# Kernel tuning notes

Measured on AMD Instinct MI355X. Metric: run time of the kernel, lower is better.

The kernel has to match this reference:

```python
import jax, jax.numpy as jnp
import numpy as np

BATCH, T, MAXLEN, DMODEL = 8, 32, 8, 256
UNITS = MAXLEN * DMODEL  # 2048, GRU units == input_dim


def setup_inputs() -> dict:
    key = jax.random.key(0)
    k1, k2, k3, k4, k5 = jax.random.split(key, 5)
    scale = 1.0 / np.sqrt(UNITS)
    x = jax.random.normal(k1, (BATCH, T, MAXLEN, DMODEL), jnp.float32)
    h0 = jax.random.normal(k2, (BATCH, UNITS), jnp.float32) * 0.1
    W = jax.random.normal(k3, (UNITS, 3 * UNITS), jnp.float32) * scale  # input kernel
    U = jax.random.normal(k4, (UNITS, 3 * UNITS), jnp.float32) * scale  # recurrent kernel
    b = jax.random.normal(k5, (2, 3 * UNITS), jnp.float32) * 0.01  # [input_bias, recurrent_bias] (reset_after)
    return {"x": x, "h0": h0, "W": W, "U": U, "b": b}


def _gru_seq(xp, h0, U, b_rec):
    """Run GRU (Keras v2, reset_after=True) over precomputed input projections.
    xp: (B, T, 3U) = x @ W + b_in ; h0: (B, U). Returns ((B,T,U) states, (B,U) last)."""
    def step(h, xp_t):
        rec = h @ U + b_rec  # (B, 3U)
        xz, xr, xh = jnp.split(xp_t, 3, axis=-1)
        rz, rr, rh = jnp.split(rec, 3, axis=-1)
        z = jax.nn.sigmoid(xz + rz)
        r = jax.nn.sigmoid(xr + rr)
        hh = jnp.tanh(xh + r * rh)
        h_new = z * h + (1.0 - z) * hh
        return h_new, h_new
    h_last, hs = jax.lax.scan(step, h0, jnp.swapaxes(xp, 0, 1))
    return jnp.swapaxes(hs, 0, 1), h_last


def reference(x, h0, W, U, b):
    # x: (B, T, M, d). Causal branch: for each mask row i, zero out positions > i
    # along the maxLen axis, run the full-sequence GRU, keep slice i of output.
    B, T, M, d = x.shape
    units = M * d
    b_in, b_rec = b[0], b[1]
    masks = jnp.tril(jnp.ones((M, M), x.dtype))  # (M, M) lower triangular
    # Fold the M mask variants into the batch dim -> one fused scan.
    xm = (x[None] * masks[:, None, None, :, None]).reshape(M * B, T, units)
    xp = jnp.einsum('bti,iu->btu', xm, W) + b_in  # precompute input projection
    h0r = jnp.broadcast_to(h0[None], (M, B, units)).reshape(M * B, units)
    hs, h_last = _gru_seq(xp, h0r, U, b_rec)
    out = hs.reshape(M, B, T, M, d)
    idx = jnp.arange(M)
    ret = out[idx, :, :, idx, :]            # (M, B, T, d): slice i of variant i
    ret = jnp.transpose(ret, (1, 2, 0, 3))  # (B, T, M, d)
    state = h_last.reshape(M, B, units)[M - 1]  # state from last (full-mask) run
    return ret, state
```

## Files before the change

### kernel.cpp

```cpp
#include <hip/hip_runtime.h>
#include <hip/hip_bf16.h>

typedef _Float16 f16x8 __attribute__((ext_vector_type(8)));
typedef float f32x4 __attribute__((ext_vector_type(4)));
typedef unsigned long long ull;

#define UNITS   2048
#define NC      6144
#define TSTEPS  32
#define HSTRIDE 131072

__device__ __forceinline__ float sigmoid_f(float v){ return 1.0f/(1.0f+__expf(-v)); }
__device__ __forceinline__ float tanh_f(float v){ return 2.0f/(1.0f+__expf(-2.0f*v)) - 1.0f; }

__global__ __launch_bounds__(256) void prep_misc(
    const float* __restrict__ x, const float* __restrict__ h0,
    _Float16* __restrict__ xh, _Float16* __restrict__ hRing,
    unsigned* __restrict__ bar)
{
  int i = blockIdx.x*256 + threadIdx.x;
  if (i < 640) bar[i] = 0;
  if (i < 524288) xh[i] = (_Float16)x[i];
  if (i < 131072) {
    int s = i >> 11, u = i & 2047;
    float v = h0[((s & 7) << 11) + u];
    hRing[(((u >> 3) << 6) + s)*8 + (u & 7)] = (_Float16)v;
  }
}

__global__ __launch_bounds__(256) void transpose_cast(
    const float* __restrict__ W, const float* __restrict__ U,
    _Float16* __restrict__ Wt, _Float16* __restrict__ Ut)
{
  __shared__ float tile[64][65];
  const float* src = blockIdx.z ? U : W;
  _Float16* dst = blockIdx.z ? Ut : Wt;
  int n0 = blockIdx.x*64, k0 = blockIdx.y*64;
  int lane = threadIdx.x & 63, grp = threadIdx.x >> 6;
  #pragma unroll
  for (int r = grp; r < 64; r += 4)
    tile[r][lane] = src[(size_t)(k0+r)*NC + n0 + lane];
  __syncthreads();
  #pragma unroll
  for (int r = grp; r < 64; r += 4)
    dst[(size_t)(n0+r)*UNITS + k0 + lane] = (_Float16)tile[lane][r];
}

__global__ __launch_bounds__(512) void xp_gemm(
    const _Float16* __restrict__ xh, const _Float16* __restrict__ Wt,
    const float* __restrict__ bin, _Float16* __restrict__ xpf)
{
  __shared__ __align__(16) short sB[64*256];
  int n0 = blockIdx.x*64, bt0 = blockIdx.y*128;
  int tid = threadIdx.x;
  int lane = tid & 63, w = tid >> 6;
  int wm = w & 3, wn = w >> 2;
  int nl = lane & 15, kg = lane >> 4;
  f32x4 acc[2][2] = {{{0,0,0,0},{0,0,0,0}},{{0,0,0,0},{0,0,0,0}}};
  for (int l = 0; l < 8; ++l) {
    __syncthreads();
    #pragma unroll
    for (int i = 0; i < 4; ++i) {
      int e = tid + i*512;
      int col = e >> 5, ch = e & 31;
      f16x8 v = *(const f16x8*)(Wt + (size_t)(n0+col)*UNITS + l*256 + ch*8);
      int off = ((col<<9) | (ch<<4)) ^ ((col&7)<<4);
      *(f16x8*)((char*)sB + off) = v;
    }
    __syncthreads();
    #pragma unroll
    for (int kk = 0; kk < 256; kk += 32) {
      f16x8 a[2];
      #pragma unroll
      for (int sub = 0; sub < 2; ++sub) {
        int row = bt0 + wm*32 + sub*16 + nl;
        a[sub] = *(const f16x8*)(xh + ((size_t)row*8 + l)*256 + kg*8 + kk);
      }
      #pragma unroll
      for (int nt = 0; nt < 2; ++nt) {
        int col = wn*32 + nt*16 + nl;
        int off = ((col<<9) | ((kk + kg*8)<<1)) ^ ((col&7)<<4);
        f16x8 bfr = *(const f16x8*)((const char*)sB + off);
        #pragma unroll
        for (int sub = 0; sub < 2; ++sub)
          acc[sub][nt] = __builtin_amdgcn_mfma_f32_16x16x32_f16(a[sub], bfr, acc[sub][nt], 0,0,0);
      }
    }
    #pragma unroll
    for (int sub = 0; sub < 2; ++sub) {
      int orow = bt0 + wm*32 + sub*16 + kg*4;
      #pragma unroll
      for (int nt = 0; nt < 2; ++nt) {
        int col = n0 + wn*32 + nt*16 + nl;
        float bv = bin[col];
        #pragma unroll
        for (int r = 0; r < 4; ++r) {
          int rr = orow + r;
          int b_ = rr >> 5, t_ = rr & 31;
          xpf[(size_t)((l*8 + b_)*32 + t_)*NC + col] = (_Float16)(acc[sub][nt][r] + bv);
        }
      }
    }
  }
}

__device__ __forceinline__ void half_barrier(unsigned* bar, int half, int idxInHalf, int t)
{
  __syncthreads();
  if (threadIdx.x == 0) {
    unsigned* grp  = bar + (half*8 + (idxInHalf & 7))*32;
    unsigned* root = bar + (16 + half)*32;
    unsigned* gen  = bar + (18 + half)*32;
    unsigned tgt = (unsigned)(t + 1);
    unsigned a = __hip_atomic_fetch_add(grp, 1u, __ATOMIC_RELAXED, __HIP_MEMORY_SCOPE_AGENT) + 1u;
    if (a == tgt*16u) {
      unsigned r = __hip_atomic_fetch_add(root, 1u, __ATOMIC_RELAXED, __HIP_MEMORY_SCOPE_AGENT) + 1u;
      if (r == tgt*8u)
        __hip_atomic_store(gen, tgt, __ATOMIC_RELEASE, __HIP_MEMORY_SCOPE_AGENT);
    }
    while (__hip_atomic_load(gen, __ATOMIC_RELAXED, __HIP_MEMORY_SCOPE_AGENT) < tgt)
      __builtin_amdgcn_s_sleep(1);
  }
  __syncthreads();
  __builtin_amdgcn_fence(__ATOMIC_ACQUIRE, "workgroup");
}

__global__ __launch_bounds__(512, 2) void gru_persist(
    const _Float16* __restrict__ Ut, const _Float16* __restrict__ xpf,
    const float* __restrict__ brec, const float* __restrict__ h0,
    _Float16* __restrict__ hRing,
    float* __restrict__ ret, float* __restrict__ st, unsigned* __restrict__ bar)
{
  __shared__ __align__(16) float sRed[48*288];

  int tid = threadIdx.x;
  int lane = tid & 63, kq = tid >> 6;
  int half = blockIdx.x & 1;
  int idxInHalf = blockIdx.x >> 1;
  int u0 = idxInHalf * 16;
  int s0 = half * 32;
  int nl = lane & 15, kg = lane >> 4;
  int redidx = lane*4 + (lane>>3)*4;

  f16x8 uw[3][8];
  #pragma unroll
  for (int g = 0; g < 3; ++g)
    #pragma unroll
    for (int kk = 0; kk < 8; ++kk) {
      uw[g][kk] = *(const f16x8*)(Ut + (size_t)(g*UNITS + u0 + nl)*UNITS + kq*256 + kk*32 + kg*8);
      asm volatile("" : "+v"(uw[g][kk]));
    }

  int s_local = tid >> 4, u_local = tid & 15;
  int sg = s0 + s_local;
  int u  = u0 + u_local;
  int mE = s_local >> 4, kgE = (s_local >> 2) & 3, rE = s_local & 3;
  int laneE = kgE*16 + u_local;
  int ridxE = laneE*4 + (laneE>>3)*4 + rE;
  int mm = u0 >> 8;

  float bz = brec[u], br = brec[2048+u], bh = brec[4096+u];
  float hprev = h0[((sg & 7) << 11) + u];

  for (int t = 0; t < TSTEPS; ++t) {
    const _Float16* hc = hRing + (size_t)t*HSTRIDE;
    _Float16*       hn = hRing + (size_t)(t+1)*HSTRIDE;

    const _Float16* xrow = xpf + ((size_t)sg*32 + t)*NC;
    float xz = (float)xrow[u];
    float xr = (float)xrow[2048+u];
    float xhv = (float)xrow[4096+u];

    f32x4 a0z={0,0,0,0}, a0r={0,0,0,0}, a0h={0,0,0,0};
    f32x4 a1z={0,0,0,0}, a1r={0,0,0,0}, a1h={0,0,0,0};
    const _Float16* Ab = hc + (size_t)(((kq*32 + kg)*64) + s0 + nl)*8;
    #pragma unroll
    for (int kk = 0; kk < 8; ++kk) {
      f16x8 av0 = *(const f16x8*)(Ab + kk*2048);
      f16x8 av1 = *(const f16x8*)(Ab + kk*2048 + 128);
      a0z = __builtin_amdgcn_mfma_f32_16x16x32_f16(av0, uw[0][kk], a0z, 0,0,0);
      a1z = __builtin_amdgcn_mfma_f32_16x16x32_f16(av1, uw[0][kk], a1z, 0,0,0);
      a0r = __builtin_amdgcn_mfma_f32_16x16x32_f16(av0, uw[1][kk], a0r, 0,0,0);
      a1r = __builtin_amdgcn_mfma_f32_16x16x32_f16(av1, uw[1][kk], a1r, 0,0,0);
      a0h = __builtin_amdgcn_mfma_f32_16x16x32_f16(av0, uw[2][kk], a0h, 0,0,0);
      a1h = __builtin_amdgcn_mfma_f32_16x16x32_f16(av1, uw[2][kk], a1h, 0,0,0);
    }

    {
      float* rp0 = &sRed[((kq*2 + 0)*3)*288 + redidx];
      *(f32x4*)(rp0)        = a0z;
      *(f32x4*)(rp0 + 288)  = a0r;
      *(f32x4*)(rp0 + 576)  = a0h;
      float* rp1 = &sRed[((kq*2 + 1)*3)*288 + redidx];
      *(f32x4*)(rp1)        = a1z;
      *(f32x4*)(rp1 + 288)  = a1r;
      *(f32x4*)(rp1 + 576)  = a1h;
    }
    __syncthreads();

    {
      float vz = 0.f, vr = 0.f, vh = 0.f;
      #pragma unroll
      for (int q = 0; q < 8; ++q) {
        const float* base = &sRed[((q*2 + mE)*3)*288 + ridxE];
        vz += base[0];
        vr += base[288];
        vh += base[576];
      }
      float z  = sigmoid_f(xz  + vz + bz);
      float rg = sigmoid_f(xr  + vr + br);
      float hh = tanh_f(xhv + rg*(vh + bh));
      float hnv = z*hprev + (1.0f - z)*hh;
      hprev = hnv;
      _Float16 hb = (_Float16)hnv;
      __hip_atomic_store((unsigned short*)hn + (size_t)(((u >> 3) << 6) + sg)*8 + (u & 7),
                         __builtin_bit_cast(unsigned short, hb),
                         __ATOMIC_RELAXED, __HIP_MEMORY_SCOPE_AGENT);
      if ((sg >> 3) == mm)
        ret[(size_t)((((sg & 7)*32 + t) << 3) + mm)*256 + (u & 255)] = hnv;
      if (t == 31 && sg >= 56)
        st[(size_t)(sg - 56)*UNITS + u] = hnv;
    }
    if (t < TSTEPS - 1)
      half_barrier(bar, half, idxInHalf, t);
  }
}

extern "C" void kernel_launch(void* const* d_in, const int* in_sizes, int n_in,
                              void* d_out, int out_size, void* d_ws, size_t ws_size,
                              hipStream_t stream) {
  const float* x  = (const float*)d_in[0];
  const float* h0 = (const float*)d_in[1];
  const float* W  = (const float*)d_in[2];
  const float* U  = (const float*)d_in[3];
  const float* b  = (const float*)d_in[4];
  float* ret = (float*)d_out;
  float* st  = ret + 524288;

  char* p = (char*)d_ws;
  _Float16* Ut = (_Float16*)p; p += 25165824;
  _Float16* Wt = (_Float16*)p; p += 25165824;
  _Float16* xh = (_Float16*)p; p += 1048576;
  _Float16* xpf = (_Float16*)p; p += 25165824;
  _Float16* hRing = (_Float16*)p; p += 33ull * HSTRIDE * 2;
  unsigned* bar = (unsigned*)p; p += 2560;

  prep_misc<<<2048, 256, 0, stream>>>(x, h0, xh, hRing, bar);
  transpose_cast<<<dim3(96,32,2), 256, 0, stream>>>(W, U, Wt, Ut);
  xp_gemm<<<dim3(96,2), 512, 0, stream>>>(xh, Wt, b, xpf);

  const float* brec = b + NC;
  void* args[] = { (void*)&Ut, (void*)&xpf, (void*)&brec, (void*)&h0,
                   (void*)&hRing, (void*)&ret, (void*)&st, (void*)&bar };
  hipLaunchCooperativeKernel((const void*)gru_persist, dim3(256), dim3(512),
                             args, 0, stream);
}
```

Measured before the change: 258.7 us.

## Replace half-grid barrier with per-wave producer flags and drop U transpose

Replaces the hierarchical per-half grid barrier with per-group counters, so each wave spins only on the 16 blocks that produce the h slice it consumes. Drops the separate U transpose/cast pass and loads fp32 U directly with strided scalar loads when filling the register-resident weights. Prefetches the next timestep's input projection before signalling. The trade-offs are weaker release ordering on the h stores (relaxed flag add with no fence) and a slower, uncoalesced weight-loading prologue.

```diff
diff --git a/kernel.cpp b/kernel.cpp
--- a/kernel.cpp
+++ b/kernel.cpp
@@ -29,21 +29,18 @@
 }
 
 __global__ __launch_bounds__(256) void transpose_cast(
-    const float* __restrict__ W, const float* __restrict__ U,
-    _Float16* __restrict__ Wt, _Float16* __restrict__ Ut)
+    const float* __restrict__ W, _Float16* __restrict__ Wt)
 {
   __shared__ float tile[64][65];
-  const float* src = blockIdx.z ? U : W;
-  _Float16* dst = blockIdx.z ? Ut : Wt;
   int n0 = blockIdx.x*64, k0 = blockIdx.y*64;
   int lane = threadIdx.x & 63, grp = threadIdx.x >> 6;
   #pragma unroll
   for (int r = grp; r < 64; r += 4)
-    tile[r][lane] = src[(size_t)(k0+r)*NC + n0 + lane];
+    tile[r][lane] = W[(size_t)(k0+r)*NC + n0 + lane];
   __syncthreads();
   #pragma unroll
   for (int r = grp; r < 64; r += 4)
-    dst[(size_t)(n0+r)*UNITS + k0 + lane] = (_Float16)tile[lane][r];
+    Wt[(size_t)(n0+r)*UNITS + k0 + lane] = (_Float16)tile[lane][r];
 }
 
 __global__ __launch_bounds__(512) void xp_gemm(
@@ -104,29 +101,9 @@
   }
 }
 
-__device__ __forceinline__ void half_barrier(unsigned* bar, int half, int idxInHalf, int t)
-{
-  __syncthreads();
-  if (threadIdx.x == 0) {
-    unsigned* grp  = bar + (half*8 + (idxInHalf & 7))*32;
-    unsigned* root = bar + (16 + half)*32;
-    unsigned* gen  = bar + (18 + half)*32;
-    unsigned tgt = (unsigned)(t + 1);
-    unsigned a = __hip_atomic_fetch_add(grp, 1u, __ATOMIC_RELAXED, __HIP_MEMORY_SCOPE_AGENT) + 1u;
-    if (a == tgt*16u) {
-      unsigned r = __hip_atomic_fetch_add(root, 1u, __ATOMIC_RELAXED, __HIP_MEMORY_SCOPE_AGENT) + 1u;
-      if (r == tgt*8u)
-        __hip_atomic_store(gen, tgt, __ATOMIC_RELEASE, __HIP_MEMORY_SCOPE_AGENT);
-    }
-    while (__hip_atomic_load(gen, __ATOMIC_RELAXED, __HIP_MEMORY_SCOPE_AGENT) < tgt)
-      __builtin_amdgcn_s_sleep(1);
-  }
-  __syncthreads();
-  __builtin_amdgcn_fence(__ATOMIC_ACQUIRE, "workgroup");
-}
-
-__global__ __launch_bounds__(512, 2) void gru_persist(
-    const _Float16* __restrict__ Ut, const _Float16* __restrict__ xpf,
+__global__ __launch_bounds__(512) __attribute__((amdgpu_waves_per_eu(2, 2)))
+void gru_persist(
+    const float* __restrict__ U, const _Float16* __restrict__ xpf,
     const float* __restrict__ brec, const float* __restrict__ h0,
     _Float16* __restrict__ hRing,
     float* __restrict__ ret, float* __restrict__ st, unsigned* __restrict__ bar)
@@ -142,12 +119,19 @@
   int nl = lane & 15, kg = lane >> 4;
   int redidx = lane*4 + (lane>>3)*4;
 
+  unsigned* myflag   = bar + (half*8 + (idxInHalf >> 4))*32;
+  const unsigned* pf = bar + (half*8 + kq)*32;
+
   f16x8 uw[3][8];
   #pragma unroll
   for (int g = 0; g < 3; ++g)
     #pragma unroll
     for (int kk = 0; kk < 8; ++kk) {
-      uw[g][kk] = *(const f16x8*)(Ut + (size_t)(g*UNITS + u0 + nl)*UNITS + kq*256 + kk*32 + kg*8);
+      f16x8 tmp;
+      #pragma unroll
+      for (int j = 0; j < 8; ++j)
+        tmp[j] = (_Float16)U[(size_t)(kq*256 + kk*32 + kg*8 + j)*NC + g*UNITS + u0 + nl];
+      uw[g][kk] = tmp;
       asm volatile("" : "+v"(uw[g][kk]));
     }
 
@@ -161,15 +145,23 @@
 
   float bz = brec[u], br = brec[2048+u], bh = brec[4096+u];
   float hprev = h0[((sg & 7) << 11) + u];
+  float xz, xr, xhv;
+  {
+    const _Float16* xrow = xpf + (size_t)sg*32*NC;
+    xz  = (float)xrow[u];
+    xr  = (float)xrow[2048+u];
+    xhv = (float)xrow[4096+u];
+  }
 
   for (int t = 0; t < TSTEPS; ++t) {
     const _Float16* hc = hRing + (size_t)t*HSTRIDE;
     _Float16*       hn = hRing + (size_t)(t+1)*HSTRIDE;
 
-    const _Float16* xrow = xpf + ((size_t)sg*32 + t)*NC;
-    float xz = (float)xrow[u];
-    float xr = (float)xrow[2048+u];
-    float xhv = (float)xrow[4096+u];
+    if (t > 0) {
+      unsigned tgt = 16u*(unsigned)t;
+      while (__hip_atomic_load(pf, __ATOMIC_RELAXED, __HIP_MEMORY_SCOPE_AGENT) < tgt) {}
+      asm volatile("" ::: "memory");
+    }
 
     f32x4 a0z={0,0,0,0}, a0r={0,0,0,0}, a0h={0,0,0,0};
     f32x4 a1z={0,0,0,0}, a1r={0,0,0,0}, a1h={0,0,0,0};
@@ -207,9 +199,9 @@
         vr += base[288];
         vh += base[576];
       }
-      float z  = sigmoid_f(xz  + vz + bz);
-      float rg = sigmoid_f(xr  + vr + br);
-      float hh = tanh_f(xhv + rg*(vh + bh));
+      float z   = sigmoid_f(xz  + vz + bz);
+      float rg  = sigmoid_f(xr  + vr + br);
+      float hh  = tanh_f(xhv + rg*(vh + bh));
       float hnv = z*hprev + (1.0f - z)*hh;
       hprev = hnv;
       _Float16 hb = (_Float16)hnv;
@@ -221,8 +213,18 @@
       if (t == 31 && sg >= 56)
         st[(size_t)(sg - 56)*UNITS + u] = hnv;
     }
-    if (t < TSTEPS - 1)
-      half_barrier(bar, half, idxInHalf, t);
+
+    if (t < TSTEPS-1) {
+      const _Float16* xrow = xpf + ((size_t)sg*32 + t + 1)*NC;
+      xz  = (float)xrow[u];
+      xr  = (float)xrow[2048+u];
+      xhv = (float)xrow[4096+u];
+    }
+
+    asm volatile("s_waitcnt vmcnt(0)" ::: "memory");
+    __syncthreads();
+    if (t < TSTEPS-1 && tid == 0)
+      __hip_atomic_fetch_add(myflag, 1u, __ATOMIC_RELAXED, __HIP_MEMORY_SCOPE_AGENT);
   }
 }
 
@@ -238,7 +240,6 @@
   float* st  = ret + 524288;
 
   char* p = (char*)d_ws;
-  _Float16* Ut = (_Float16*)p; p += 25165824;
   _Float16* Wt = (_Float16*)p; p += 25165824;
   _Float16* xh = (_Float16*)p; p += 1048576;
   _Float16* xpf = (_Float16*)p; p += 25165824;
@@ -246,11 +247,11 @@
   unsigned* bar = (unsigned*)p; p += 2560;
 
   prep_misc<<<2048, 256, 0, stream>>>(x, h0, xh, hRing, bar);
-  transpose_cast<<<dim3(96,32,2), 256, 0, stream>>>(W, U, Wt, Ut);
+  transpose_cast<<<dim3(96,32), 256, 0, stream>>>(W, Wt);
   xp_gemm<<<dim3(96,2), 512, 0, stream>>>(xh, Wt, b, xpf);
 
   const float* brec = b + NC;
-  void* args[] = { (void*)&Ut, (void*)&xpf, (void*)&brec, (void*)&h0,
+  void* args[] = { (void*)&U, (void*)&xpf, (void*)&brec, (void*)&h0,
                    (void*)&hRing, (void*)&ret, (void*)&st, (void*)&bar };
   hipLaunchCooperativeKernel((const void*)gru_persist, dim3(256), dim3(512),
                              args, 0, stream);
```

Measured after the change: 292.4 us. 13.0% more time.

## Flatten grid barrier, prefetch next-step inputs, defer output stores past barrier

Applied to the files above, without the earlier changes.

The two-level barrier (group counters, root counter, generation flag) becomes one level: each block bumps its group counter and thread 0 polls all eight group counters until every one reaches the target, removing the serial root-counter hop. The next step's input projections are loaded after the barrier, and the ret/state stores are moved after it too, taking that global traffic off the critical path before signalling. An explicit vmcnt wait makes the h stores complete before arrival. The U-weight registers are constrained to AGPRs to relieve VGPR pressure, which may add copies if the MFMA operands have to move back to VGPRs.

```diff
diff --git a/kernel.cpp b/kernel.cpp
--- a/kernel.cpp
+++ b/kernel.cpp
@@ -108,18 +108,20 @@
 {
   __syncthreads();
   if (threadIdx.x == 0) {
-    unsigned* grp  = bar + (half*8 + (idxInHalf & 7))*32;
-    unsigned* root = bar + (16 + half)*32;
-    unsigned* gen  = bar + (18 + half)*32;
-    unsigned tgt = (unsigned)(t + 1);
-    unsigned a = __hip_atomic_fetch_add(grp, 1u, __ATOMIC_RELAXED, __HIP_MEMORY_SCOPE_AGENT) + 1u;
-    if (a == tgt*16u) {
-      unsigned r = __hip_atomic_fetch_add(root, 1u, __ATOMIC_RELAXED, __HIP_MEMORY_SCOPE_AGENT) + 1u;
-      if (r == tgt*8u)
-        __hip_atomic_store(gen, tgt, __ATOMIC_RELEASE, __HIP_MEMORY_SCOPE_AGENT);
-    }
-    while (__hip_atomic_load(gen, __ATOMIC_RELAXED, __HIP_MEMORY_SCOPE_AGENT) < tgt)
+    unsigned* grp = bar + (half*8 + (idxInHalf & 7))*32;
+    __hip_atomic_fetch_add(grp, 1u, __ATOMIC_RELAXED, __HIP_MEMORY_SCOPE_AGENT);
+    const unsigned* base = bar + half*8*32;
+    unsigned tgt = 16u*(unsigned)(t + 1);
+    for (;;) {
+      unsigned mn = 0xffffffffu;
+      #pragma unroll
+      for (int g = 0; g < 8; ++g) {
+        unsigned v = __hip_atomic_load(base + g*32, __ATOMIC_RELAXED, __HIP_MEMORY_SCOPE_AGENT);
+        mn = v < mn ? v : mn;
+      }
+      if (mn >= tgt) break;
       __builtin_amdgcn_s_sleep(1);
+    }
   }
   __syncthreads();
   __builtin_amdgcn_fence(__ATOMIC_ACQUIRE, "workgroup");
@@ -148,7 +150,7 @@
     #pragma unroll
     for (int kk = 0; kk < 8; ++kk) {
       uw[g][kk] = *(const f16x8*)(Ut + (size_t)(g*UNITS + u0 + nl)*UNITS + kq*256 + kk*32 + kg*8);
-      asm volatile("" : "+v"(uw[g][kk]));
+      asm volatile("" : "+a"(uw[g][kk]));
     }
 
   int s_local = tid >> 4, u_local = tid & 15;
@@ -161,15 +163,17 @@
 
   float bz = brec[u], br = brec[2048+u], bh = brec[4096+u];
   float hprev = h0[((sg & 7) << 11) + u];
+  float xz, xr, xhv;
+  {
+    const _Float16* xrow = xpf + (size_t)sg*32*NC;
+    xz  = (float)xrow[u];
+    xr  = (float)xrow[2048+u];
+    xhv = (float)xrow[4096+u];
+  }
 
   for (int t = 0; t < TSTEPS; ++t) {
     const _Float16* hc = hRing + (size_t)t*HSTRIDE;
     _Float16*       hn = hRing + (size_t)(t+1)*HSTRIDE;
-
-    const _Float16* xrow = xpf + ((size_t)sg*32 + t)*NC;
-    float xz = (float)xrow[u];
-    float xr = (float)xrow[2048+u];
-    float xhv = (float)xrow[4096+u];
 
     f32x4 a0z={0,0,0,0}, a0r={0,0,0,0}, a0h={0,0,0,0};
     f32x4 a1z={0,0,0,0}, a1r={0,0,0,0}, a1h={0,0,0,0};
@@ -198,6 +202,7 @@
     }
     __syncthreads();
 
+    float hnv;
     {
       float vz = 0.f, vr = 0.f, vh = 0.f;
       #pragma unroll
@@ -207,22 +212,31 @@
         vr += base[288];
         vh += base[576];
       }
-      float z  = sigmoid_f(xz  + vz + bz);
-      float rg = sigmoid_f(xr  + vr + br);
-      float hh = tanh_f(xhv + rg*(vh + bh));
-      float hnv = z*hprev + (1.0f - z)*hh;
+      float z   = sigmoid_f(xz  + vz + bz);
+      float rg  = sigmoid_f(xr  + vr + br);
+      float hh  = tanh_f(xhv + rg*(vh + bh));
+      hnv = z*hprev + (1.0f - z)*hh;
       hprev = hnv;
       _Float16 hb = (_Float16)hnv;
       __hip_atomic_store((unsigned short*)hn + (size_t)(((u >> 3) << 6) + sg)*8 + (u & 7),
                          __builtin_bit_cast(unsigned short, hb),
                          __ATOMIC_RELAXED, __HIP_MEMORY_SCOPE_AGENT);
-      if ((sg >> 3) == mm)
-        ret[(size_t)((((sg & 7)*32 + t) << 3) + mm)*256 + (u & 255)] = hnv;
-      if (t == 31 && sg >= 56)
-        st[(size_t)(sg - 56)*UNITS + u] = hnv;
-    }
+    }
+    asm volatile("s_waitcnt vmcnt(0)" ::: "memory");
+
     if (t < TSTEPS - 1)
       half_barrier(bar, half, idxInHalf, t);
+
+    if ((sg >> 3) == mm)
+      ret[(size_t)((((sg & 7)*32 + t) << 3) + mm)*256 + (u & 255)] = hnv;
+    if (t == 31 && sg >= 56)
+      st[(size_t)(sg - 56)*UNITS + u] = hnv;
+    if (t < TSTEPS - 1) {
+      const _Float16* xrow = xpf + ((size_t)sg*32 + t + 1)*NC;
+      xz  = (float)xrow[u];
+      xr  = (float)xrow[2048+u];
+      xhv = (float)xrow[4096+u];
+    }
   }
 }
 
```

Result: slower. 269.5 us (+4.2%).

## Replace grid-wide half barrier with per-slice dataflow flags for GRU steps

Applied to the files above, without the earlier changes.

Replaces the hierarchical per-half grid barrier with per-K-slice counters. Each block bumps the counter for the group of units it produces, and each wave spins only on the counter for the K slice it consumes. This lets blocks start the next step as soon as their needed inputs are ready instead of waiting for all blocks, and it moves the ret/st output stores after the signal so they leave the critical path. The risk is memory-ordering: the code relies on relaxed atomics plus an explicit vmcnt wait, with no acquire/release fences, and spinning without sleep adds pressure on the atomic unit.

```diff
diff --git a/kernel.cpp b/kernel.cpp
--- a/kernel.cpp
+++ b/kernel.cpp
@@ -104,27 +104,6 @@
   }
 }
 
-__device__ __forceinline__ void half_barrier(unsigned* bar, int half, int idxInHalf, int t)
-{
-  __syncthreads();
-  if (threadIdx.x == 0) {
-    unsigned* grp  = bar + (half*8 + (idxInHalf & 7))*32;
-    unsigned* root = bar + (16 + half)*32;
-    unsigned* gen  = bar + (18 + half)*32;
-    unsigned tgt = (unsigned)(t + 1);
-    unsigned a = __hip_atomic_fetch_add(grp, 1u, __ATOMIC_RELAXED, __HIP_MEMORY_SCOPE_AGENT) + 1u;
-    if (a == tgt*16u) {
-      unsigned r = __hip_atomic_fetch_add(root, 1u, __ATOMIC_RELAXED, __HIP_MEMORY_SCOPE_AGENT) + 1u;
-      if (r == tgt*8u)
-        __hip_atomic_store(gen, tgt, __ATOMIC_RELEASE, __HIP_MEMORY_SCOPE_AGENT);
-    }
-    while (__hip_atomic_load(gen, __ATOMIC_RELAXED, __HIP_MEMORY_SCOPE_AGENT) < tgt)
-      __builtin_amdgcn_s_sleep(1);
-  }
-  __syncthreads();
-  __builtin_amdgcn_fence(__ATOMIC_ACQUIRE, "workgroup");
-}
-
 __global__ __launch_bounds__(512, 2) void gru_persist(
     const _Float16* __restrict__ Ut, const _Float16* __restrict__ xpf,
     const float* __restrict__ brec, const float* __restrict__ h0,
@@ -142,6 +121,9 @@
   int nl = lane & 15, kg = lane >> 4;
   int redidx = lane*4 + (lane>>3)*4;
 
+  unsigned* myflag   = bar + (half*8 + (idxInHalf >> 4))*32;
+  const unsigned* pf = bar + (half*8 + kq)*32;
+
   f16x8 uw[3][8];
   #pragma unroll
   for (int g = 0; g < 3; ++g)
@@ -166,9 +148,15 @@
     const _Float16* hc = hRing + (size_t)t*HSTRIDE;
     _Float16*       hn = hRing + (size_t)(t+1)*HSTRIDE;
 
+    if (t > 0) {
+      unsigned tgt = 16u*(unsigned)t;
+      while (__hip_atomic_load(pf, __ATOMIC_RELAXED, __HIP_MEMORY_SCOPE_AGENT) < tgt) {}
+      asm volatile("" ::: "memory");
+    }
+
     const _Float16* xrow = xpf + ((size_t)sg*32 + t)*NC;
-    float xz = (float)xrow[u];
-    float xr = (float)xrow[2048+u];
+    float xz  = (float)xrow[u];
+    float xr  = (float)xrow[2048+u];
     float xhv = (float)xrow[4096+u];
 
     f32x4 a0z={0,0,0,0}, a0r={0,0,0,0}, a0h={0,0,0,0};
@@ -198,6 +186,7 @@
     }
     __syncthreads();
 
+    float hnv;
     {
       float vz = 0.f, vr = 0.f, vh = 0.f;
       #pragma unroll
@@ -207,22 +196,25 @@
         vr += base[288];
         vh += base[576];
       }
-      float z  = sigmoid_f(xz  + vz + bz);
-      float rg = sigmoid_f(xr  + vr + br);
-      float hh = tanh_f(xhv + rg*(vh + bh));
-      float hnv = z*hprev + (1.0f - z)*hh;
+      float z   = sigmoid_f(xz  + vz + bz);
+      float rg  = sigmoid_f(xr  + vr + br);
+      float hh  = tanh_f(xhv + rg*(vh + bh));
+      hnv = z*hprev + (1.0f - z)*hh;
       hprev = hnv;
       _Float16 hb = (_Float16)hnv;
       __hip_atomic_store((unsigned short*)hn + (size_t)(((u >> 3) << 6) + sg)*8 + (u & 7),
                          __builtin_bit_cast(unsigned short, hb),
                          __ATOMIC_RELAXED, __HIP_MEMORY_SCOPE_AGENT);
-      if ((sg >> 3) == mm)
-        ret[(size_t)((((sg & 7)*32 + t) << 3) + mm)*256 + (u & 255)] = hnv;
-      if (t == 31 && sg >= 56)
-        st[(size_t)(sg - 56)*UNITS + u] = hnv;
-    }
-    if (t < TSTEPS - 1)
-      half_barrier(bar, half, idxInHalf, t);
+    }
+    asm volatile("s_waitcnt vmcnt(0)" ::: "memory");
+    __syncthreads();
+    if (t < TSTEPS-1 && tid == 0)
+      __hip_atomic_fetch_add(myflag, 1u, __ATOMIC_RELAXED, __HIP_MEMORY_SCOPE_AGENT);
+
+    if ((sg >> 3) == mm)
+      ret[(size_t)((((sg & 7)*32 + t) << 3) + mm)*256 + (u & 255)] = hnv;
+    if (t == 31 && sg >= 56)
+      st[(size_t)(sg - 56)*UNITS + u] = hnv;
   }
 }
 
```

Measured after the change: 355.6 us. +37.5%, slower.
